# Kernel tuning notes

Measured on AMD Instinct MI355X. Metric: run time of the kernel, lower is better.

## Reference

```python
import jax, jax.numpy as jnp
import numpy as np

EPS = 1e-6  # flax nn.LayerNorm default epsilon


def excl_cumsum(a, axis):
    c = jnp.roll(jnp.cumsum(a, axis=axis), 1, axis=axis)
    idx = [slice(None)] * a.ndim
    idx[axis] = slice(0, 1)
    return c.at[tuple(idx)].set(0.0)


def mixed_chunk_attn(q, k, v, n_chunks):
    # Mixed chunk linear attention (https://arxiv.org/pdf/2202.10447.pdf)
    if n_chunks == 1:
        mask = jnp.tri(q.shape[1], q.shape[1], -1, dtype=q.dtype)
        qk = jnp.einsum('bls,bms->blm', q, k) * mask
        return jnp.einsum('blm,bme->ble', qk, v)
    B, L = q.shape[:2]
    C = L // n_chunks
    qc = q.reshape(B, n_chunks, C, -1)
    kc = k.reshape(B, n_chunks, C, -1)
    vc = v.reshape(B, n_chunks, C, -1)
    # global linear attention across chunks (exclusive prefix of kv states)
    kv = excl_cumsum(jnp.einsum('bgcs,bgce->bgse', kc, vc), axis=1)
    glob = jnp.einsum('bgcs,bgse->bgce', qc, kv)
    # local strictly-causal quadratic attention within each chunk
    mask = jnp.tri(C, C, -1, dtype=q.dtype)
    qk = jnp.einsum('bgns,bgms->bgnm', qc, kc) * mask
    loc = jnp.einsum('bgnm,bgme->bgne', qk, vc)
    return (glob + loc).reshape(B, L, -1)


def ln_normalize(x):
    mu = jnp.mean(x, axis=-1, keepdims=True)
    var = jnp.mean(jnp.square(x - mu), axis=-1, keepdims=True)
    return (x - mu) * jax.lax.rsqrt(var + EPS)


def fwblock(x, labels, weights, W1, b1, W2, b2, ln_scale, ln_bias, Wu, bu, step_sizes, n_chunks):
    B, L, D = x.shape
    F = W1.shape[1]

    # slow-weight forward with zero perturbations; grad wrt perturbations gives
    # per-token gradients at each layer's output (rank-one fast-weight updates).
    def slow_loss(p1, p3, p_scale, p_bias):
        h1 = x @ W1 + b1 + p1                    # FWDense(4D) + output perturbation
        h2 = jnp.square(jax.nn.relu(h1))         # FWSquaredRelu (paramless)
        h3 = h2 @ W2 + b2 + p3                   # FWDense(D) + output perturbation
        h4 = ln_normalize(h3) * (ln_scale + p_scale) + (ln_bias + p_bias)
        logits = h4 @ Wu + bu
        ll = -jnp.sum(jax.nn.log_softmax(logits) * labels, axis=-1)
        loss = jnp.sum(weights * ll) / jnp.maximum(jnp.sum(weights), 1e-8)
        return loss, h2

    zeros = (jnp.zeros((B, L, F), x.dtype), jnp.zeros((B, L, D), x.dtype),
             jnp.zeros((B, L, D), x.dtype), jnp.zeros((B, L, D), x.dtype))
    (g1, g3, g_scale, g_bias), h2_slow = jax.grad(
        slow_loss, argnums=(0, 1, 2, 3), has_aux=True)(*zeros)

    # fast-weight forward: rank-one weight updates expressed as causal linear attn
    x1 = x @ W1 + b1 - step_sizes[0] * mixed_chunk_attn(x, x, g1, n_chunks)
    x2 = jnp.square(jax.nn.relu(x1))             # step_sizes[1] unused (no params)
    x3 = x2 @ W2 + b2 - step_sizes[2] * mixed_chunk_attn(x2, h2_slow, g3, n_chunks)
    fast_scale = ln_scale - step_sizes[3] * excl_cumsum(g_scale, axis=1)
    fast_bias = ln_bias - step_sizes[3] * excl_cumsum(g_bias, axis=1)
    x4 = ln_normalize(x3) * fast_scale + fast_bias
    return x4 @ Wu + bu


def setup_inputs():
    key = jax.random.key(0)
    ks = jax.random.split(key, 6)
    B, L, D, V = 2, 2048, 1024, 8192
    F = 4 * D
    x = jax.random.normal(ks[0], (B, L, D), jnp.float32)
    labels = jax.random.uniform(ks[1], (B, L, V), jnp.float32)
    weights = jnp.ones((B, L), jnp.float32)
    W1 = jax.random.normal(ks[2], (D, F), jnp.float32) / np.sqrt(D).astype(np.float32)
    b1 = jnp.zeros((F,), jnp.float32)
    W2 = jax.random.normal(ks[3], (F, D), jnp.float32) / np.sqrt(F).astype(np.float32)
    b2 = jnp.zeros((D,), jnp.float32)
    ln_scale = jnp.ones((D,), jnp.float32)
    ln_bias = jnp.zeros((D,), jnp.float32)
    Wu = jax.random.normal(ks[4], (D, V), jnp.float32) / np.sqrt(D).astype(np.float32)
    bu = jnp.zeros((V,), jnp.float32)
    step_sizes = jnp.full((4,), 0.01, jnp.float32)
    return dict(x=x, labels=labels, weights=weights, W1=W1, b1=b1, W2=W2, b2=b2,
                ln_scale=ln_scale, ln_bias=ln_bias, Wu=Wu, bu=bu,
                step_sizes=step_sizes, n_chunks=16)


def reference(x, labels, weights, W1, b1, W2, b2, ln_scale, ln_bias, Wu, bu, step_sizes, n_chunks):
    return fwblock(x, labels, weights, W1, b1, W2, b2, ln_scale, ln_bias, Wu, bu, step_sizes, n_chunks)
```

## Files before the change

kernel.cpp:

```cpp
#include <hip/hip_runtime.h>
#include <cstdint>

typedef unsigned short ushort_t;
typedef __bf16 bf16x8 __attribute__((ext_vector_type(8)));
typedef float f32x4 __attribute__((ext_vector_type(4)));

__device__ __forceinline__ ushort_t f2bf(float f) {
  union { float f; unsigned int u; } v; v.f = f;
  unsigned int u = v.u;
  unsigned int r = (u + 0x7fffu + ((u >> 16) & 1u)) >> 16;
  return (ushort_t)r;
}
__device__ __forceinline__ float bf2f(ushort_t u) {
  union { unsigned int u; float f; } v; v.u = ((unsigned int)u) << 16; return v.f;
}

#define GLOAD16(gp, lp)                                                              \
  __builtin_amdgcn_global_load_lds(                                                  \
      reinterpret_cast<const __attribute__((address_space(1))) unsigned int*>(       \
          reinterpret_cast<uintptr_t>(gp)),                                          \
      reinterpret_cast<__attribute__((address_space(3))) unsigned int*>(             \
          reinterpret_cast<uintptr_t>(lp)),                                          \
      16, 0, 0)

struct GemmP {
  const ushort_t* A; const ushort_t* B;
  int M, N, K;
  long long sA, sB;
  float* outf;   long long sOutF;
  ushort_t* outb; long long sOutB;
  ushort_t* outb2;
  const float* bias;
  const float* auxf; long long sAuxF;
  const ushort_t* auxb;
  const float* steps;
  float* part; int ksplit, Kc, Tt;
};

template <int EPI>
__global__ __launch_bounds__(512, 2) void gemm256(GemmP p) {
  const int nwg = gridDim.x * gridDim.y;
  const int orig = blockIdx.y * gridDim.x + blockIdx.x;
  const int xcd = orig & 7, loc = orig >> 3;
  const int q8 = nwg >> 3, r8 = nwg & 7;
  const int wg = (xcd < r8) ? (xcd * (q8 + 1) + loc) : (r8 * (q8 + 1) + (xcd - r8) * q8 + loc);
  int mt, nt;
  if (EPI == 7) {
    int t_ = wg;
    mt = (int)((sqrtf(8.f * t_ + 1.f) - 1.f) * 0.5f);
    while ((mt + 1) * (mt + 2) / 2 <= t_) mt++;
    while (mt * (mt + 1) / 2 > t_) mt--;
    nt = t_ - mt * (mt + 1) / 2;
  } else {
    nt = wg % gridDim.x; mt = wg / gridDim.x;
  }
  const int m0 = mt * 256, n0 = nt * 256;

  int bz = blockIdx.z, ks = 0;
  if (EPI == 6 || EPI == 7) { bz = blockIdx.z / p.ksplit; ks = blockIdx.z % p.ksplit; }

  const ushort_t* A = p.A + (size_t)bz * p.sA;
  const ushort_t* B = p.B + (size_t)bz * p.sB;

  int kbeg = 0, kend = p.K;
  if (EPI == 6 || EPI == 7) { kbeg = ks * p.Kc; kend = kbeg + p.Kc; }
  else if (EPI == 4) kend = min(p.K, m0 + 256);

  extern __shared__ ushort_t smem[];
  ushort_t* sA = smem;
  ushort_t* sB = smem + 3 * 8192;

  const int tid = threadIdx.x;
  const int wid = tid >> 6, lane = tid & 63;
  const int wm = wid >> 2, wn = wid & 3;

  f32x4 acc[8][4];
#pragma unroll
  for (int i = 0; i < 8; i++)
#pragma unroll
    for (int j = 0; j < 4; j++) acc[i][j] = f32x4{0.f, 0.f, 0.f, 0.f};

  const int lr = lane >> 2;
  const int lcsw = (((lane & 3) ^ ((lr >> 1) & 3)) * 8);
  const int rT0 = wid * 16 + lr;
  const int rT1 = 128 + wid * 16 + lr;
  const ushort_t* gA0 = A + (size_t)(m0 + rT0) * p.K + lcsw;
  const ushort_t* gA1 = A + (size_t)(m0 + rT1) * p.K + lcsw;
  const ushort_t* gB0 = B + (size_t)(n0 + rT0) * p.K + lcsw;
  const ushort_t* gB1 = B + (size_t)(n0 + rT1) * p.K + lcsw;
  ushort_t* lA0 = &sA[wid * 512];
  ushort_t* lA1 = &sA[(8 + wid) * 512];
  ushort_t* lB0 = &sB[wid * 512];
  ushort_t* lB1 = &sB[(8 + wid) * 512];

  const int fr = lane & 15;
  const int q = lane >> 4;
  const int slot = (q ^ ((fr >> 1) & 3)) * 8;
  int offA[8], offB[4];
#pragma unroll
  for (int i = 0; i < 8; i++) offA[i] = (wm * 8 + i) * 512 + fr * 32 + slot;
#pragma unroll
  for (int j = 0; j < 4; j++) offB[j] = (wn * 4 + j) * 512 + fr * 32 + slot;

  const int nIter = (kend - kbeg) >> 5;
  auto stage = [&](int t, int buf) {
    const int kk = kbeg + t * 32;
    const int o = buf * 8192;
    GLOAD16(gA0 + kk, lA0 + o);
    GLOAD16(gA1 + kk, lA1 + o);
    GLOAD16(gB0 + kk, lB0 + o);
    GLOAD16(gB1 + kk, lB1 + o);
  };
  stage(0, 0);
  if (nIter > 1) stage(1, 1);

  for (int t = 0; t < nIter; ++t) {
    if (t + 1 < nIter) { asm volatile("s_waitcnt vmcnt(4)" ::: "memory"); }
    else               { asm volatile("s_waitcnt vmcnt(0)" ::: "memory"); }
    __builtin_amdgcn_s_barrier();
    __builtin_amdgcn_sched_barrier(0);
    if (t + 2 < nIter) stage(t + 2, (t + 2) % 3);
    const int co = (t % 3) * 8192;
    bf16x8 av[8], bv[4];
#pragma unroll
    for (int j = 0; j < 4; j++) bv[j] = *reinterpret_cast<const bf16x8*>(&sB[co + offB[j]]);
#pragma unroll
    for (int i = 0; i < 8; i++) {
      av[i] = *reinterpret_cast<const bf16x8*>(&sA[co + offA[i]]);
#pragma unroll
      for (int j = 0; j < 4; j++)
        acc[i][j] = __builtin_amdgcn_mfma_f32_16x16x32_bf16(av[i], bv[j], acc[i][j], 0, 0, 0);
    }
  }

  const int fq = q;
  float ss = 0.f;
  if (EPI == 4) ss = p.steps[0];
  float* outf = p.outf ? p.outf + (size_t)bz * p.sOutF : nullptr;
  ushort_t* outb = p.outb ? p.outb + (size_t)bz * p.sOutB : nullptr;
  ushort_t* outb2 = p.outb2;
  const ushort_t* auxb = p.auxb ? p.auxb + (size_t)bz * p.sAuxF : nullptr;
  float* partT = nullptr;
  if (EPI == 6) partT = p.part + (size_t)blockIdx.z * p.M * p.N;
  if (EPI == 7) partT = p.part + ((size_t)blockIdx.z * p.Tt + wg) * 65536;

#pragma unroll
  for (int i = 0; i < 8; i++) {
#pragma unroll
    for (int j = 0; j < 4; j++) {
#pragma unroll
      for (int r2 = 0; r2 < 4; r2++) {
        int lrow = wm * 128 + i * 16 + fq * 4 + r2;
        int lcol = wn * 64 + j * 16 + fr;
        int row = m0 + lrow, col = n0 + lcol;
        size_t g = (size_t)row * p.N + col;
        float v = acc[i][j][r2];
        if (EPI == 0) {
          outf[g] = v + (p.bias ? p.bias[col] : 0.f);
        } else if (EPI == 8) {
          outb[g] = f2bf(v + p.bias[col]);
        } else if (EPI == 1) {
          v += p.bias[col];
          outb[g] = f2bf(v);
          float rl = fmaxf(v, 0.f);
          outb2[g] = f2bf(rl * rl);
        } else if (EPI == 2) {
          outb[g] = f2bf(v * 2.f * sqrtf(bf2f(auxb[g])));
        } else if (EPI == 4) {
          float x1 = bf2f(auxb[g]) - ss * v;
          float rl = fmaxf(x1, 0.f);
          outb[g] = f2bf(rl * rl);
        } else if (EPI == 6) {
          partT[g] = v;
        } else if (EPI == 7) {
          partT[lrow * 256 + lcol] = v;
        }
      }
    }
  }
}

template <int EPI>
__global__ __launch_bounds__(256) void gemm_bt(GemmP p) {
  const int nwg = gridDim.x * gridDim.y;
  const int orig = blockIdx.y * gridDim.x + blockIdx.x;
  const int xcd = orig & 7, loc = orig >> 3;
  const int q = nwg >> 3, r = nwg & 7;
  const int wg = (xcd < r) ? (xcd * (q + 1) + loc) : (r * (q + 1) + (xcd - r) * q + loc);
  const int nt = wg % gridDim.x, mt = wg / gridDim.x;
  const int m0 = mt * 128, n0 = nt * 128;
  const int bz = blockIdx.z;

  const ushort_t* A = p.A + (size_t)bz * p.sA;
  const ushort_t* B = p.B + (size_t)bz * p.sB;

  int kend = p.K;
  if (EPI == 5) kend = min(p.K, m0 + 128);

  __shared__ ushort_t sA[3 * 128 * 32];
  __shared__ ushort_t sB[3 * 128 * 32];

  const int tid = threadIdx.x;
  const int wid = tid >> 6, lane = tid & 63;
  const int wm = wid >> 1, wn = wid & 1;

  f32x4 acc[4][4];
#pragma unroll
  for (int i = 0; i < 4; i++)
#pragma unroll
    for (int j = 0; j < 4; j++) acc[i][j] = f32x4{0.f, 0.f, 0.f, 0.f};

  const int lr = lane >> 2;
  const int lc = (lane & 3) * 8;
  const int rA0 = wid * 16 + lr;
  const int rA1 = 64 + wid * 16 + lr;
  const ushort_t* gA0 = A + (size_t)(m0 + rA0) * p.K + lc;
  const ushort_t* gA1 = A + (size_t)(m0 + rA1) * p.K + lc;
  const ushort_t* gB0 = B + (size_t)(n0 + rA0) * p.K + lc;
  const ushort_t* gB1 = B + (size_t)(n0 + rA1) * p.K + lc;
  ushort_t* lA0 = &sA[wid * 512];
  ushort_t* lA1 = &sA[(4 + wid) * 512];
  ushort_t* lB0 = &sB[wid * 512];
  ushort_t* lB1 = &sB[(4 + wid) * 512];

  const int fr = lane & 15;
  const int kb = (lane >> 4) * 8;

  const int nIter = kend >> 5;
  auto stage = [&](int t, int buf) {
    const int kk = t * 32;
    const int o = buf * 4096;
    GLOAD16(gA0 + kk, lA0 + o);
    GLOAD16(gA1 + kk, lA1 + o);
    GLOAD16(gB0 + kk, lB0 + o);
    GLOAD16(gB1 + kk, lB1 + o);
  };
  stage(0, 0);
  if (nIter > 1) stage(1, 1);

  for (int t = 0; t < nIter; ++t) {
    if (t + 1 < nIter) { asm volatile("s_waitcnt vmcnt(4)" ::: "memory"); }
    else               { asm volatile("s_waitcnt vmcnt(0)" ::: "memory"); }
    __builtin_amdgcn_s_barrier();
    __builtin_amdgcn_sched_barrier(0);
    if (t + 2 < nIter) stage(t + 2, (t + 2) % 3);
    const int co = (t % 3) * 4096;
    bf16x8 av[4], bv[4];
#pragma unroll
    for (int i = 0; i < 4; i++) {
      av[i] = *reinterpret_cast<const bf16x8*>(&sA[co + (wm * 64 + i * 16 + fr) * 32 + kb]);
      bv[i] = *reinterpret_cast<const bf16x8*>(&sB[co + (wn * 64 + i * 16 + fr) * 32 + kb]);
    }
#pragma unroll
    for (int i = 0; i < 4; i++)
#pragma unroll
      for (int j = 0; j < 4; j++)
        acc[i][j] = __builtin_amdgcn_mfma_f32_16x16x32_bf16(av[i], bv[j], acc[i][j], 0, 0, 0);
  }

  const int fq = lane >> 4;
  float ss = (EPI == 5) ? p.steps[2] : 0.f;
  float* outf = p.outf ? p.outf + (size_t)bz * p.sOutF : nullptr;
  const float* auxf = p.auxf ? p.auxf + (size_t)bz * p.sAuxF : nullptr;

#pragma unroll
  for (int i = 0; i < 4; i++) {
#pragma unroll
    for (int j = 0; j < 4; j++) {
#pragma unroll
      for (int r2 = 0; r2 < 4; r2++) {
        int row = m0 + wm * 64 + i * 16 + fq * 4 + r2;
        int col = n0 + wn * 64 + j * 16 + fr;
        size_t g = (size_t)row * p.N + col;
        float v = acc[i][j][r2];
        if (EPI == 5) {
          outf[g] = auxf[g] - ss * v;
        } else {
          outf[g] = v + (p.bias ? p.bias[col] : 0.f);
        }
      }
    }
  }
}

__global__ __launch_bounds__(256) void k_comb(const float* part, const float* bias, float* out,
                                              int N, size_t MN, int S) {
  size_t e = ((size_t)blockIdx.x * 256 + threadIdx.x) * 4;
  if (e >= MN) return;
  float4 s = *(const float4*)(part + e);
  for (int p_ = 1; p_ < S; p_++) {
    float4 v = *(const float4*)(part + (size_t)p_ * MN + e);
    s.x += v.x; s.y += v.y; s.z += v.z; s.w += v.w;
  }
  if (bias) {
    int col = (int)(e % (size_t)N);
    s.x += bias[col]; s.y += bias[col + 1]; s.z += bias[col + 2]; s.w += bias[col + 3];
  }
  *(float4*)(out + e) = s;
}

__global__ __launch_bounds__(256) void k_combtri(const float* part, ushort_t* out, int Tt, int S,
                                                 int L) {
  int t = blockIdx.x, bz = blockIdx.y;
  int mt = (int)((sqrtf(8.f * t + 1.f) - 1.f) * 0.5f);
  while ((mt + 1) * (mt + 2) / 2 <= t) mt++;
  while (mt * (mt + 1) / 2 > t) mt--;
  int nt = t - mt * (mt + 1) / 2;
  const float* pb = part + ((size_t)bz * S * Tt + t) * 65536;
  ushort_t* ob = out + (size_t)bz * L * L;
  for (int e4 = threadIdx.x; e4 < 16384; e4 += 256) {
    int e = e4 * 4;
    float4 s = *(const float4*)(pb + e);
    for (int p_ = 1; p_ < S; p_++) {
      float4 v = *(const float4*)(pb + (size_t)p_ * Tt * 65536 + e);
      s.x += v.x; s.y += v.y; s.z += v.z; s.w += v.w;
    }
    int lr = e >> 8, lc2 = e & 255;
    int row = mt * 256 + lr, col = nt * 256 + lc2;
    ushort4 o;
    o.x = (col < row) ? f2bf(s.x) : (ushort_t)0;
    o.y = (col + 1 < row) ? f2bf(s.y) : (ushort_t)0;
    o.z = (col + 2 < row) ? f2bf(s.z) : (ushort_t)0;
    o.w = (col + 3 < row) ? f2bf(s.w) : (ushort_t)0;
    *(ushort4*)(&ob[(size_t)row * L + col]) = o;
  }
}

__global__ __launch_bounds__(256) void k_conv(const float* in, ushort_t* out, size_t n) {
  size_t i = ((size_t)blockIdx.x * 256 + threadIdx.x) * 4;
  if (i >= n) return;
  float4 v = *(const float4*)(in + i);
  out[i] = f2bf(v.x); out[i + 1] = f2bf(v.y); out[i + 2] = f2bf(v.z); out[i + 3] = f2bf(v.w);
}

__global__ __launch_bounds__(256) void k_tconv(const float* in, ushort_t* out, int R, int C) {
  __shared__ float t[32][33];
  int c0 = blockIdx.x * 32, r0 = blockIdx.y * 32;
  int tx = threadIdx.x & 31, ty = threadIdx.x >> 5;
#pragma unroll
  for (int i = ty; i < 32; i += 8) t[i][tx] = in[(size_t)(r0 + i) * C + c0 + tx];
  __syncthreads();
#pragma unroll
  for (int i = ty; i < 32; i += 8) out[(size_t)(c0 + i) * R + r0 + tx] = f2bf(t[tx][i]);
}

__global__ __launch_bounds__(256) void k_tb2b(const ushort_t* in, ushort_t* out, int L, int C) {
  __shared__ ushort_t t[32][33];
  int b = blockIdx.z;
  const ushort_t* ib = in + (size_t)b * L * C;
  ushort_t* ob = out + (size_t)b * C * L;
  int c0 = blockIdx.x * 32, l0 = blockIdx.y * 32;
  int tx = threadIdx.x & 31, ty = threadIdx.x >> 5;
#pragma unroll
  for (int i = ty; i < 32; i += 8) t[i][tx] = ib[(size_t)(l0 + i) * C + c0 + tx];
  __syncthreads();
#pragma unroll
  for (int i = ty; i < 32; i += 8) ob[(size_t)(c0 + i) * L + l0 + tx] = t[tx][i];
}

__device__ __forceinline__ void blockRed2(float& a, float& b, float* red) {
#pragma unroll
  for (int o = 32; o; o >>= 1) { a += __shfl_down(a, o); b += __shfl_down(b, o); }
  int w = threadIdx.x >> 6;
  if ((threadIdx.x & 63) == 0) { red[w] = a; red[4 + w] = b; }
  __syncthreads();
  a = red[0] + red[1] + red[2] + red[3];
  b = red[4] + red[5] + red[6] + red[7];
  __syncthreads();
}

__global__ __launch_bounds__(256) void k_lnfwd(const float* X, const float* sc, const float* bi,
                                               float* nout, float* rstd, ushort_t* yb, int D) {
  __shared__ float red[8];
  int row = blockIdx.x;
  const float* x = X + (size_t)row * D;
  float s = 0.f, s2 = 0.f;
  for (int d = threadIdx.x; d < D; d += 256) { float v = x[d]; s += v; s2 += v * v; }
  blockRed2(s, s2, red);
  float mu = s / D;
  float var = s2 / D - mu * mu;
  float rs = rsqrtf(var + 1e-6f);
  for (int d = threadIdx.x; d < D; d += 256) {
    float nv = (x[d] - mu) * rs;
    nout[(size_t)row * D + d] = nv;
    yb[(size_t)row * D + d] = f2bf(nv * sc[d] + bi[d]);
  }
  if (threadIdx.x == 0) rstd[row] = rs;
}

__global__ __launch_bounds__(256) void k_lnfwd2(const float* X, const float* fs, const float* fb,
                                                ushort_t* yb, int D) {
  __shared__ float red[8];
  int row = blockIdx.x;
  const float* x = X + (size_t)row * D;
  float s = 0.f, s2 = 0.f;
  for (int d = threadIdx.x; d < D; d += 256) { float v = x[d]; s += v; s2 += v * v; }
  blockRed2(s, s2, red);
  float mu = s / D;
  float var = s2 / D - mu * mu;
  float rs = rsqrtf(var + 1e-6f);
  for (int d = threadIdx.x; d < D; d += 256) {
    size_t g = (size_t)row * D + d;
    float nv = (x[d] - mu) * rs;
    yb[g] = f2bf(nv * fs[g] + fb[g]);
  }
}

__global__ __launch_bounds__(256) void k_lnbwd(const float* G, const float* nn, const float* rstd,
                                               const float* sc, ushort_t* g3b, float* gsc, int D) {
  __shared__ float red[8];
  int row = blockIdx.x;
  const float* g = G + (size_t)row * D;
  const float* n_ = nn + (size_t)row * D;
  float sa = 0.f, sb = 0.f;
  for (int d = threadIdx.x; d < D; d += 256) {
    float dn = g[d] * sc[d];
    sa += dn; sb += dn * n_[d];
  }
  blockRed2(sa, sb, red);
  float a = sa / D, b = sb / D, rs = rstd[row];
  for (int d = threadIdx.x; d < D; d += 256) {
    size_t gi = (size_t)row * D + d;
    float dn = g[d] * sc[d];
    g3b[gi] = f2bf(rs * (dn - a - n_[d] * b));
    gsc[gi] = g[d] * n_[d];
  }
}

__global__ __launch_bounds__(256) void k_wsum(const float* w, float* o, int n) {
  __shared__ float red[4];
  float s = 0.f;
  for (int i = threadIdx.x; i < n; i += 256) s += w[i];
#pragma unroll
  for (int d = 32; d; d >>= 1) s += __shfl_down(s, d);
  if ((threadIdx.x & 63) == 0) red[threadIdx.x >> 6] = s;
  __syncthreads();
  if (threadIdx.x == 0) o[0] = fmaxf(red[0] + red[1] + red[2] + red[3], 1e-8f);
}

__global__ __launch_bounds__(256) void k_softgrad(const ushort_t* logits, const float* labels,
                                                  const float* w, const float* wsum,
                                                  ushort_t* dlb, int V) {
  __shared__ float lrow[8192];
  __shared__ float red[8];
  int row = blockIdx.x;
  const ushort_t* l = logits + (size_t)row * V;
  const float* y = labels + (size_t)row * V;
  float m = -3.4e38f, t = 0.f;
  for (int v = threadIdx.x; v < V; v += 256) {
    float lv = bf2f(l[v]);
    lrow[v] = lv;
    m = fmaxf(m, lv);
    t += y[v];
  }
#pragma unroll
  for (int o = 32; o; o >>= 1) { m = fmaxf(m, __shfl_down(m, o)); t += __shfl_down(t, o); }
  int wv = threadIdx.x >> 6;
  if ((threadIdx.x & 63) == 0) { red[wv] = m; red[4 + wv] = t; }
  __syncthreads();
  m = fmaxf(fmaxf(red[0], red[1]), fmaxf(red[2], red[3]));
  t = red[4] + red[5] + red[6] + red[7];
  __syncthreads();
  float s = 0.f;
  for (int v = threadIdx.x; v < V; v += 256) s += expf(lrow[v] - m);
#pragma unroll
  for (int o = 32; o; o >>= 1) s += __shfl_down(s, o);
  if ((threadIdx.x & 63) == 0) red[wv] = s;
  __syncthreads();
  s = red[0] + red[1] + red[2] + red[3];
  float c = w[row] / wsum[0];
  float invs = 1.f / s;
  for (int v = threadIdx.x; v < V; v += 256) {
    size_t g = (size_t)row * V + v;
    dlb[g] = f2bf(c * (expf(lrow[v] - m) * invs * t - y[v]));
  }
}

__global__ __launch_bounds__(256) void k_scanpart(const float* gs, const float* gb, float* ps,
                                                  float* pb, int L, int D) {
  int d = blockIdx.x * 256 + threadIdx.x;
  int seg = blockIdx.y, b = blockIdx.z;
  const int SEGL = L / 16;
  size_t base = ((size_t)b * L + seg * SEGL) * D + d;
  float s1 = 0.f, s2 = 0.f;
  for (int i = 0; i < SEGL; i++) { s1 += gs[base + (size_t)i * D]; s2 += gb[base + (size_t)i * D]; }
  size_t pi = ((size_t)b * 16 + seg) * D + d;
  ps[pi] = s1; pb[pi] = s2;
}

__global__ __launch_bounds__(256) void k_scanapply(const float* gs, const float* gb,
                                                   const float* ps, const float* pb,
                                                   const float* sc, const float* bi,
                                                   const float* steps, float* fs, float* fb,
                                                   int L, int D) {
  int d = blockIdx.x * 256 + threadIdx.x;
  int seg = blockIdx.y, b = blockIdx.z;
  const int SEGL = L / 16;
  float ss = steps[3];
  float rs_ = 0.f, rb_ = 0.f;
  for (int s = 0; s < seg; s++) {
    size_t pi = ((size_t)b * 16 + s) * D + d;
    rs_ += ps[pi]; rb_ += pb[pi];
  }
  float s0 = sc[d], b0 = bi[d];
  size_t base = ((size_t)b * L + seg * SEGL) * D + d;
  for (int i = 0; i < SEGL; i++) {
    size_t g = base + (size_t)i * D;
    fs[g] = s0 - ss * rs_;
    fb[g] = b0 - ss * rb_;
    rs_ += gs[g]; rb_ += gb[g];
  }
}

extern "C" void kernel_launch(void* const* d_in, const int* in_sizes, int n_in, void* d_out,
                              int out_size, void* d_ws, size_t ws_size, hipStream_t stream) {
  const float* x        = (const float*)d_in[0];
  const float* labels   = (const float*)d_in[1];
  const float* weights  = (const float*)d_in[2];
  const float* W1       = (const float*)d_in[3];
  const float* b1       = (const float*)d_in[4];
  const float* W2       = (const float*)d_in[5];
  const float* b2       = (const float*)d_in[6];
  const float* ln_scale = (const float*)d_in[7];
  const float* ln_bias  = (const float*)d_in[8];
  const float* Wu       = (const float*)d_in[9];
  const float* bu       = (const float*)d_in[10];
  const float* steps    = (const float*)d_in[11];

  const int BL = in_sizes[2];
  const int D  = in_sizes[7];
  const int F  = in_sizes[4];
  const int V  = in_sizes[10];
  const int Bb = 2, L = BL / Bb;
  const int T2t = (L / 256) * (L / 256 + 1) / 2;
  const unsigned SMEM = 3 * 8192 * 2 * 2;

  char* ws = (char*)d_ws;
  size_t off = 0;
  auto take = [&](size_t b) { char* p = ws + off; off = (off + b + 255) & ~(size_t)255; return p; };

  ushort_t* xb   = (ushort_t*)take((size_t)BL * D * 2);
  ushort_t* w1t  = (ushort_t*)take((size_t)F * D * 2);
  ushort_t* w2t  = (ushort_t*)take((size_t)D * F * 2);
  ushort_t* w2b  = (ushort_t*)take((size_t)F * D * 2);
  ushort_t* wut  = (ushort_t*)take((size_t)V * D * 2);
  ushort_t* wub  = (ushort_t*)take((size_t)D * V * 2);
  ushort_t* H1b  = (ushort_t*)take((size_t)BL * F * 2);
  ushort_t* H2b  = (ushort_t*)take((size_t)BL * F * 2);
  float*    H3   = (float*)take((size_t)BL * D * 4);
  float*    nbuf = (float*)take((size_t)BL * D * 4);
  float*    rstd = (float*)take((size_t)BL * 4);
  ushort_t* h4b  = (ushort_t*)take((size_t)BL * D * 2);
  float*    wsumb= (float*)take(256);
  float*    G4   = (float*)take((size_t)BL * D * 4);
  float*    gsc  = (float*)take((size_t)BL * D * 4);
  ushort_t* g3b  = (ushort_t*)take((size_t)BL * D * 2);
  ushort_t* g3t  = (ushort_t*)take((size_t)BL * D * 2);
  float*    fs   = (float*)take((size_t)BL * D * 4);
  float*    fb   = (float*)take((size_t)BL * D * 4);
  ushort_t* x4b  = (ushort_t*)take((size_t)BL * D * 2);
  float*    psc  = (float*)take((size_t)Bb * 16 * D * 4);
  float*    pbi  = (float*)take((size_t)Bb * 16 * D * 4);
  char* poolA = take((size_t)BL * V * 4);
  ushort_t* logitsb = (ushort_t*)poolA;
  float*    partA  = (float*)poolA;
  ushort_t* g1b = (ushort_t*)poolA;
  ushort_t* g1t = (ushort_t*)(poolA + (size_t)BL * F * 2);
  ushort_t* S1b = (ushort_t*)(poolA + (size_t)BL * F * 4);
  ushort_t* x2b = (ushort_t*)(poolA + (size_t)BL * F * 4 + (size_t)Bb * L * L * 2);
  char* poolB = take((size_t)BL * V * 2);
  ushort_t* dlb = (ushort_t*)poolB;
  float*    partS1 = (float*)poolB;
  ushort_t* S2b = (ushort_t*)poolB;
  float*    X3  = (float*)(poolB + (size_t)Bb * L * L * 2);
  float*    x3  = (float*)(poolB + (size_t)Bb * L * L * 2 + (size_t)BL * D * 4);

  dim3 blk(256), blk5(512);
  const size_t MN_D = (size_t)BL * D;

  k_conv<<<dim3((unsigned)((size_t)BL * D / 1024)), blk, 0, stream>>>(x, xb, (size_t)BL * D);
  k_tconv<<<dim3(F / 32, D / 32), blk, 0, stream>>>(W1, w1t, D, F);
  k_tconv<<<dim3(D / 32, F / 32), blk, 0, stream>>>(W2, w2t, F, D);
  k_conv<<<dim3((unsigned)((size_t)F * D / 1024)), blk, 0, stream>>>(W2, w2b, (size_t)F * D);
  k_tconv<<<dim3(V / 32, D / 32), blk, 0, stream>>>(Wu, wut, D, V);
  k_conv<<<dim3((unsigned)((size_t)D * V / 1024)), blk, 0, stream>>>(Wu, wub, (size_t)D * V);

  GemmP p;
  auto clr = [&]() { p = GemmP{}; };

  clr(); p.A = xb; p.B = w1t; p.M = BL; p.N = F; p.K = D;
  p.outb = H1b; p.outb2 = H2b; p.bias = b1;
  gemm256<1><<<dim3(F / 256, BL / 256, 1), blk5, SMEM, stream>>>(p);
  clr(); p.A = H2b; p.B = w2t; p.M = BL; p.N = D; p.K = F;
  p.part = partA; p.ksplit = 4; p.Kc = F / 4;
  gemm256<6><<<dim3(D / 256, BL / 256, 4), blk5, SMEM, stream>>>(p);
  k_comb<<<dim3((unsigned)(MN_D / 1024)), blk, 0, stream>>>(partA, b2, H3, D, MN_D, 4);
  k_lnfwd<<<dim3(BL), blk, 0, stream>>>(H3, ln_scale, ln_bias, nbuf, rstd, h4b, D);
  clr(); p.A = h4b; p.B = wut; p.M = BL; p.N = V; p.K = D; p.outb = logitsb; p.bias = bu;
  gemm256<8><<<dim3(V / 256, BL / 256, 1), blk5, SMEM, stream>>>(p);
  k_wsum<<<dim3(1), blk, 0, stream>>>(weights, wsumb, BL);
  k_softgrad<<<dim3(BL), blk, 0, stream>>>(logitsb, labels, weights, wsumb, dlb, V);
  clr(); p.A = dlb; p.B = wub; p.M = BL; p.N = D; p.K = V;
  p.part = partA; p.ksplit = 4; p.Kc = V / 4;
  gemm256<6><<<dim3(D / 256, BL / 256, 4), blk5, SMEM, stream>>>(p);
  k_comb<<<dim3((unsigned)(MN_D / 1024)), blk, 0, stream>>>(partA, nullptr, G4, D, MN_D, 4);
  k_lnbwd<<<dim3(BL), blk, 0, stream>>>(G4, nbuf, rstd, ln_scale, g3b, gsc, D);
  clr(); p.A = g3b; p.B = w2b; p.M = BL; p.N = F; p.K = D; p.outb = g1b; p.auxb = H2b;
  gemm256<2><<<dim3(F / 256, BL / 256, 1), blk5, SMEM, stream>>>(p);
  k_tb2b<<<dim3(F / 32, L / 32, Bb), blk, 0, stream>>>(g1b, g1t, L, F);
  k_tb2b<<<dim3(D / 32, L / 32, Bb), blk, 0, stream>>>(g3b, g3t, L, D);
  clr(); p.A = xb; p.B = xb; p.M = L; p.N = L; p.K = D;
  p.sA = (long long)L * D; p.sB = (long long)L * D;
  p.part = partS1; p.ksplit = 2; p.Kc = D / 2; p.Tt = T2t;
  gemm256<7><<<dim3(T2t, 1, Bb * 2), blk5, SMEM, stream>>>(p);
  k_combtri<<<dim3(T2t, Bb), blk, 0, stream>>>(partS1, S1b, T2t, 2, L);
  clr(); p.A = S1b; p.B = g1t; p.M = L; p.N = F; p.K = L;
  p.sA = (long long)L * L; p.sB = (long long)F * L;
  p.outb = x2b; p.sOutB = (long long)L * F; p.auxb = H1b; p.sAuxF = (long long)L * F;
  p.steps = steps;
  gemm256<4><<<dim3(F / 256, L / 256, Bb), blk5, SMEM, stream>>>(p);
  clr(); p.A = x2b; p.B = w2t; p.M = BL; p.N = D; p.K = F;
  p.part = partA; p.ksplit = 4; p.Kc = F / 4;
  gemm256<6><<<dim3(D / 256, BL / 256, 4), blk5, SMEM, stream>>>(p);
  k_comb<<<dim3((unsigned)(MN_D / 1024)), blk, 0, stream>>>(partA, b2, X3, D, MN_D, 4);
  clr(); p.A = x2b; p.B = H2b; p.M = L; p.N = L; p.K = F;
  p.sA = (long long)L * F; p.sB = (long long)L * F;
  p.part = partA; p.ksplit = 4; p.Kc = F / 4; p.Tt = T2t;
  gemm256<7><<<dim3(T2t, 1, Bb * 4), blk5, SMEM, stream>>>(p);
  k_combtri<<<dim3(T2t, Bb), blk, 0, stream>>>(partA, S2b, T2t, 4, L);
  clr(); p.A = S2b; p.B = g3t; p.M = L; p.N = D; p.K = L;
  p.sA = (long long)L * L; p.sB = (long long)D * L;
  p.outf = x3; p.sOutF = (long long)L * D; p.auxf = X3; p.sAuxF = (long long)L * D; p.steps = steps;
  gemm_bt<5><<<dim3(D / 128, L / 128, Bb), blk, 0, stream>>>(p);
  k_scanpart<<<dim3(D / 256, 16, Bb), blk, 0, stream>>>(gsc, G4, psc, pbi, L, D);
  k_scanapply<<<dim3(D / 256, 16, Bb), blk, 0, stream>>>(gsc, G4, psc, pbi, ln_scale, ln_bias,
                                                         steps, fs, fb, L, D);
  k_lnfwd2<<<dim3(BL), blk, 0, stream>>>(x3, fs, fb, x4b, D);
  clr(); p.A = x4b; p.B = wut; p.M = BL; p.N = V; p.K = D; p.outf = (float*)d_out; p.bias = bu;
  gemm256<0><<<dim3(V / 256, BL / 256, 1), blk5, SMEM, stream>>>(p);
}
```

Measured before the change: 1.157 ms.

## Fuse weight cast/transpose, fold split-K combine into LayerNorm, vectorize softmax grad

```diff
diff --git a/kernel.cpp b/kernel.cpp
--- a/kernel.cpp
+++ b/kernel.cpp
@@ -4,6 +4,7 @@
 typedef unsigned short ushort_t;
 typedef __bf16 bf16x8 __attribute__((ext_vector_type(8)));
 typedef float f32x4 __attribute__((ext_vector_type(4)));
+typedef ushort_t us8 __attribute__((ext_vector_type(8)));
 
 __device__ __forceinline__ ushort_t f2bf(float f) {
   union { float f; unsigned int u; } v; v.f = f;
@@ -344,6 +345,25 @@
   for (int i = ty; i < 32; i += 8) out[(size_t)(c0 + i) * R + r0 + tx] = f2bf(t[tx][i]);
 }
 
+__global__ __launch_bounds__(256) void k_wprep(const float* in, ushort_t* outS, ushort_t* outT,
+                                               int R, int C) {
+  __shared__ float t[32][33];
+  int c0 = blockIdx.x * 32, r0 = blockIdx.y * 32;
+  int tx = threadIdx.x & 31, ty = threadIdx.x >> 5;
+#pragma unroll
+  for (int i = ty; i < 32; i += 8) {
+    float v = in[(size_t)(r0 + i) * C + c0 + tx];
+    t[i][tx] = v;
+    outS[(size_t)(r0 + i) * C + c0 + tx] = f2bf(v);
+  }
+  __syncthreads();
+#pragma unroll
+  for (int i = ty; i < 32; i += 8) out:
+  ;
+#pragma unroll
+  for (int i = ty; i < 32; i += 8) outT[(size_t)(c0 + i) * R + r0 + tx] = f2bf(t[tx][i]);
+}
+
 __global__ __launch_bounds__(256) void k_tb2b(const ushort_t* in, ushort_t* out, int L, int C) {
   __shared__ ushort_t t[32][33];
   int b = blockIdx.z;
@@ -369,22 +389,38 @@
   __syncthreads();
 }
 
-__global__ __launch_bounds__(256) void k_lnfwd(const float* X, const float* sc, const float* bi,
-                                               float* nout, float* rstd, ushort_t* yb, int D) {
+__global__ __launch_bounds__(256) void k_lncomb(const float* part, const float* bias,
+                                                const float* sc, const float* bi, float* nout,
+                                                float* rstd, ushort_t* yb, size_t MN, int D,
+                                                int S) {
   __shared__ float red[8];
   int row = blockIdx.x;
-  const float* x = X + (size_t)row * D;
-  float s = 0.f, s2 = 0.f;
-  for (int d = threadIdx.x; d < D; d += 256) { float v = x[d]; s += v; s2 += v * v; }
-  blockRed2(s, s2, red);
-  float mu = s / D;
+  int d = threadIdx.x * 4;
+  size_t g = (size_t)row * D + d;
+  float4 v = *(const float4*)(part + g);
+  for (int s_ = 1; s_ < S; s_++) {
+    float4 w = *(const float4*)(part + (size_t)s_ * MN + g);
+    v.x += w.x; v.y += w.y; v.z += w.z; v.w += w.w;
+  }
+  float4 bb = *(const float4*)(bias + d);
+  v.x += bb.x; v.y += bb.y; v.z += bb.z; v.w += bb.w;
+  float s1 = v.x + v.y + v.z + v.w;
+  float s2 = v.x * v.x + v.y * v.y + v.z * v.z + v.w * v.w;
+  blockRed2(s1, s2, red);
+  float mu = s1 / D;
   float var = s2 / D - mu * mu;
   float rs = rsqrtf(var + 1e-6f);
-  for (int d = threadIdx.x; d < D; d += 256) {
-    float nv = (x[d] - mu) * rs;
-    nout[(size_t)row * D + d] = nv;
-    yb[(size_t)row * D + d] = f2bf(nv * sc[d] + bi[d]);
-  }
+  float4 nv;
+  nv.x = (v.x - mu) * rs; nv.y = (v.y - mu) * rs; nv.z = (v.z - mu) * rs; nv.w = (v.w - mu) * rs;
+  *(float4*)(nout + g) = nv;
+  float4 scv = *(const float4*)(sc + d);
+  float4 biv = *(const float4*)(bi + d);
+  ushort4 o;
+  o.x = f2bf(nv.x * scv.x + biv.x);
+  o.y = f2bf(nv.y * scv.y + biv.y);
+  o.z = f2bf(nv.z * scv.z + biv.z);
+  o.w = f2bf(nv.w * scv.w + biv.w);
+  *(ushort4*)(yb + g) = o;
   if (threadIdx.x == 0) rstd[row] = rs;
 }
 
@@ -441,38 +477,51 @@
 __global__ __launch_bounds__(256) void k_softgrad(const ushort_t* logits, const float* labels,
                                                   const float* w, const float* wsum,
                                                   ushort_t* dlb, int V) {
-  __shared__ float lrow[8192];
   __shared__ float red[8];
-  int row = blockIdx.x;
-  const ushort_t* l = logits + (size_t)row * V;
-  const float* y = labels + (size_t)row * V;
-  float m = -3.4e38f, t = 0.f;
-  for (int v = threadIdx.x; v < V; v += 256) {
-    float lv = bf2f(l[v]);
-    lrow[v] = lv;
-    m = fmaxf(m, lv);
-    t += y[v];
-  }
+  const int row = blockIdx.x;
+  const int tid = threadIdx.x;
+  const ushort_t* l = logits + (size_t)row * V + tid * 32;
+  const float* y = labels + (size_t)row * V + tid * 32;
+  float lv[32], yv[32];
+#pragma unroll
+  for (int i = 0; i < 4; i++) {
+    us8 u = *reinterpret_cast<const us8*>(l + i * 8);
+#pragma unroll
+    for (int j = 0; j < 8; j++) lv[i * 8 + j] = bf2f(u[j]);
+  }
+#pragma unroll
+  for (int i = 0; i < 8; i++) {
+    float4 v = *reinterpret_cast<const float4*>(y + i * 4);
+    yv[i * 4] = v.x; yv[i * 4 + 1] = v.y; yv[i * 4 + 2] = v.z; yv[i * 4 + 3] = v.w;
+  }
+  float m = lv[0], t = yv[0];
+#pragma unroll
+  for (int i = 1; i < 32; i++) { m = fmaxf(m, lv[i]); t += yv[i]; }
 #pragma unroll
   for (int o = 32; o; o >>= 1) { m = fmaxf(m, __shfl_down(m, o)); t += __shfl_down(t, o); }
-  int wv = threadIdx.x >> 6;
-  if ((threadIdx.x & 63) == 0) { red[wv] = m; red[4 + wv] = t; }
+  int wv = tid >> 6;
+  if ((tid & 63) == 0) { red[wv] = m; red[4 + wv] = t; }
   __syncthreads();
   m = fmaxf(fmaxf(red[0], red[1]), fmaxf(red[2], red[3]));
   t = red[4] + red[5] + red[6] + red[7];
   __syncthreads();
   float s = 0.f;
-  for (int v = threadIdx.x; v < V; v += 256) s += expf(lrow[v] - m);
+#pragma unroll
+  for (int i = 0; i < 32; i++) { lv[i] = expf(lv[i] - m); s += lv[i]; }
 #pragma unroll
   for (int o = 32; o; o >>= 1) s += __shfl_down(s, o);
-  if ((threadIdx.x & 63) == 0) red[wv] = s;
+  if ((tid & 63) == 0) red[wv] = s;
   __syncthreads();
   s = red[0] + red[1] + red[2] + red[3];
   float c = w[row] / wsum[0];
-  float invs = 1.f / s;
-  for (int v = threadIdx.x; v < V; v += 256) {
-    size_t g = (size_t)row * V + v;
-    dlb[g] = f2bf(c * (expf(lrow[v] - m) * invs * t - y[v]));
+  float ci = c * t / s;
+  ushort_t* dl = dlb + (size_t)row * V + tid * 32;
+#pragma unroll
+  for (int i = 0; i < 4; i++) {
+    us8 o;
+#pragma unroll
+    for (int j = 0; j < 8; j++) o[j] = f2bf(ci * lv[i * 8 + j] - c * yv[i * 8 + j]);
+    *reinterpret_cast<us8*>(dl + i * 8) = o;
   }
 }
 
@@ -547,7 +596,6 @@
   ushort_t* wub  = (ushort_t*)take((size_t)D * V * 2);
   ushort_t* H1b  = (ushort_t*)take((size_t)BL * F * 2);
   ushort_t* H2b  = (ushort_t*)take((size_t)BL * F * 2);
-  float*    H3   = (float*)take((size_t)BL * D * 4);
   float*    nbuf = (float*)take((size_t)BL * D * 4);
   float*    rstd = (float*)take((size_t)BL * 4);
   ushort_t* h4b  = (ushort_t*)take((size_t)BL * D * 2);
@@ -580,10 +628,8 @@
 
   k_conv<<<dim3((unsigned)((size_t)BL * D / 1024)), blk, 0, stream>>>(x, xb, (size_t)BL * D);
   k_tconv<<<dim3(F / 32, D / 32), blk, 0, stream>>>(W1, w1t, D, F);
-  k_tconv<<<dim3(D / 32, F / 32), blk, 0, stream>>>(W2, w2t, F, D);
-  k_conv<<<dim3((unsigned)((size_t)F * D / 1024)), blk, 0, stream>>>(W2, w2b, (size_t)F * D);
-  k_tconv<<<dim3(V / 32, D / 32), blk, 0, stream>>>(Wu, wut, D, V);
-  k_conv<<<dim3((unsigned)((size_t)D * V / 1024)), blk, 0, stream>>>(Wu, wub, (size_t)D * V);
+  k_wprep<<<dim3(D / 32, F / 32), blk, 0, stream>>>(W2, w2b, w2t, F, D);
+  k_wprep<<<dim3(V / 32, D / 32), blk, 0, stream>>>(Wu, wub, wut, D, V);
 
   GemmP p;
   auto clr = [&]() { p = GemmP{}; };
@@ -594,8 +640,7 @@
   clr(); p.A = H2b; p.B = w2t; p.M = BL; p.N = D; p.K = F;
   p.part = partA; p.ksplit = 4; p.Kc = F / 4;
   gemm256<6><<<dim3(D / 256, BL / 256, 4), blk5, SMEM, stream>>>(p);
-  k_comb<<<dim3((unsigned)(MN_D / 1024)), blk, 0, stream>>>(partA, b2, H3, D, MN_D, 4);
-  k_lnfwd<<<dim3(BL), blk, 0, stream>>>(H3, ln_scale, ln_bias, nbuf, rstd, h4b, D);
+  k_lncomb<<<dim3(BL), blk, 0, stream>>>(partA, b2, ln_scale, ln_bias, nbuf, rstd, h4b, MN_D, D, 4);
   clr(); p.A = h4b; p.B = wut; p.M = BL; p.N = V; p.K = D; p.outb = logitsb; p.bias = bu;
   gemm256<8><<<dim3(V / 256, BL / 256, 1), blk5, SMEM, stream>>>(p);
   k_wsum<<<dim3(1), blk, 0, stream>>>(weights, wsumb, BL);
```

Measured after the change: 1.083 ms. 1.07x faster.
